# Performance work log

Hardware: AMD Instinct MI355X
Metric: run time of the kernel (lower is better)

## Reference

```python
import jax, jax.numpy as jnp
import numpy as np


def setup_inputs() -> dict:
    key = jax.random.key(0)
    k1, k2, k3, k4 = jax.random.split(key, 4)
    B, N, F, H, O = 4, 2048, 256, 8, 256
    nodes = jax.random.normal(k1, (B, N, F), dtype=jnp.float32)
    W_heads = jax.random.normal(k2, (H, F, F), dtype=jnp.float32) * (1.0 / np.sqrt(F))
    W_out = jax.random.normal(k3, (H * F, O), dtype=jnp.float32) * (1.0 / np.sqrt(H * F))
    bias = jax.random.normal(k4, (O,), dtype=jnp.float32) * 0.02
    return {"nodes": nodes, "W_heads": W_heads, "W_out": W_out, "bias": bias}


def reference(nodes, W_heads, W_out, bias):
    # nodes: [B,N,F]; W_heads: [H,F,F]; W_out: [H*F,O]; bias: [O]
    B, N, F = nodes.shape
    H = W_heads.shape[0]
    norm = 1.0 / jnp.sqrt(jnp.asarray(F, dtype=nodes.dtype))
    # per-head bilinear scores: (x @ W_h) @ x^T  -> [B,H,N,N]
    xw = jnp.einsum('bnf,hfg->bhng', nodes, W_heads)
    scores = jnp.einsum('bhng,bmg->bhnm', xw, nodes) * norm
    att = jax.nn.softmax(scores, axis=-1)
    # messages: att @ x (V = input nodes) -> [B,H,N,F]
    msgs = jnp.einsum('bhnm,bmf->bhnf', att, nodes)
    # concat heads along feature axis (head 0 first) -> [B,N,H*F]
    msgs = msgs.transpose(0, 2, 1, 3).reshape(B, N, H * F)
    return jnp.matmul(msgs, W_out) + bias
```

## Files before the change

kernel.cpp:

```cpp
#include <hip/hip_runtime.h>
#include <hip/hip_bf16.h>

#define B_ 4
#define N_ 2048
#define F_ 256
#define H_ 8
#define O_ 256

#define SCALE_QK 0.09016844005556021f

typedef __attribute__((ext_vector_type(8))) short short8;
typedef __attribute__((ext_vector_type(4))) short s16x4;
typedef __attribute__((ext_vector_type(4))) float f32x4;
typedef __attribute__((ext_vector_type(4))) unsigned int u32x4;

static __device__ __forceinline__ float bf2f(short u) {
    unsigned int x = ((unsigned int)(unsigned short)u) << 16;
    return __builtin_bit_cast(float, x);
}
static __device__ __forceinline__ short f2bf(float f) {
    unsigned int x = __builtin_bit_cast(unsigned int, f);
    unsigned int lsb = (x >> 16) & 1u;
    x += 0x7fffu + lsb;
    return (short)(x >> 16);
}
static __device__ __forceinline__ unsigned int pkbf(float a, float b) {
    return (unsigned int)(unsigned short)f2bf(a) |
           ((unsigned int)(unsigned short)f2bf(b) << 16);
}

static __device__ __forceinline__ void gld16(const short* g, short* l) {
    __builtin_amdgcn_global_load_lds(
        (const __attribute__((address_space(1))) void*)g,
        (__attribute__((address_space(3))) void*)l, 16, 0, 0);
}

__global__ __launch_bounds__(256) void cvtT_kernel(const float* __restrict__ src,
                                                   short* __restrict__ dst,
                                                   int R, int C) {
    __shared__ short tile[32][33];
    src += (size_t)blockIdx.z * R * C;
    dst += (size_t)blockIdx.z * R * C;
    int tx = threadIdx.x, ty = threadIdx.y;
    int c0 = blockIdx.x * 32, r0 = blockIdx.y * 32;
#pragma unroll
    for (int j = 0; j < 4; j++) {
        int r = r0 + ty + j * 8;
        tile[ty + j * 8][tx] = f2bf(src[(size_t)r * C + c0 + tx]);
    }
    __syncthreads();
#pragma unroll
    for (int j = 0; j < 4; j++) {
        int c = c0 + ty + j * 8;
        dst[(size_t)c * R + r0 + tx] = tile[tx][ty + j * 8];
    }
}

__global__ __launch_bounds__(256) void cvt_kernel(const float* __restrict__ src,
                                                  short* __restrict__ dst, int n) {
    int i = blockIdx.x * 256 + threadIdx.x;
    if (n >= 2048) {
        size_t base = (size_t)i * 8;
#pragma unroll
        for (int j = 0; j < 8; j++) dst[base + j] = f2bf(src[base + j]);
    } else if (i < n) {
        dst[i] = f2bf(src[i]);
    }
}

template <int NCT>
__device__ __forceinline__ void gemm64_bt(const short* __restrict__ A, int lda,
                                          const short* __restrict__ Bt, int ldb,
                                          float* __restrict__ C, int ldc,
                                          int K, const short* __restrict__ bias) {
    __shared__ short sA[64][72];
    __shared__ short sB[NCT * 16][72];
    int tid = threadIdx.x;
    int w = tid >> 6, l = tid & 63, lq = l & 15, quad = l >> 4;
    f32x4 acc[NCT];
#pragma unroll
    for (int i = 0; i < NCT; i++) acc[i] = (f32x4)(0.f);

    for (int kb = 0; kb < K; kb += 64) {
        __syncthreads();
#pragma unroll
        for (int i = 0; i < 2; i++) {
            int idx = tid + i * 256; int r = idx >> 3, c = (idx & 7) * 8;
            *(short8*)&sA[r][c] = *(const short8*)&A[(size_t)r * lda + kb + c];
        }
#pragma unroll
        for (int i = 0; i < NCT / 2; i++) {
            int idx = tid + i * 256; int r = idx >> 3, c = (idx & 7) * 8;
            *(short8*)&sB[r][c] = *(const short8*)&Bt[(size_t)r * ldb + kb + c];
        }
        __syncthreads();
#pragma unroll
        for (int kk = 0; kk < 2; kk++) {
            short8 af = *(const short8*)&sA[w * 16 + lq][kk * 32 + quad * 8];
#pragma unroll
            for (int ct = 0; ct < NCT; ct++) {
                short8 bf = *(const short8*)&sB[ct * 16 + lq][kk * 32 + quad * 8];
                acc[ct] = __builtin_amdgcn_mfma_f32_16x16x32_bf16(af, bf, acc[ct], 0, 0, 0);
            }
        }
    }
#pragma unroll
    for (int ct = 0; ct < NCT; ct++) {
        int col = ct * 16 + lq;
        float bv = bias ? bf2f(bias[col]) : 0.f;
#pragma unroll
        for (int r = 0; r < 4; r++) {
            int row = w * 16 + quad * 4 + r;
            C[(size_t)row * ldc + col] = acc[ct][r] + bv;
        }
    }
}

__global__ __launch_bounds__(256) void out_kernel(const short* __restrict__ msgs,
                                                  const short* __restrict__ WoutT,
                                                  const short* __restrict__ bias,
                                                  float* __restrict__ out) {
    int mt = blockIdx.x, nt = blockIdx.y;
    gemm64_bt<4>(msgs + (size_t)mt * 64 * (H_ * F_), H_ * F_,
                 WoutT + (size_t)nt * 64 * (H_ * F_), H_ * F_,
                 out + (size_t)mt * 64 * O_ + nt * 64, O_,
                 H_ * F_, bias + nt * 64);
}


#define STAGE_KV(KT, KVF, KVTF) do {                                         \
    _Pragma("unroll")                                                        \
    for (int i_ = 0; i_ < 4; i_++) {                                         \
        int rk_ = w * 8 + i_ * 2 + (l >> 5);                                 \
        int bk_ = (l & 31) ^ (rk_ & 31);                                     \
        gld16(&Xb[(size_t)((KT) * 64 + rk_) * F_ + bk_ * 8],                 \
              &KVF[(w * 8 + i_ * 2) * 256]);                                 \
        int rt_ = w * 32 + i_ * 8 + (l >> 3);                                \
        int bt_ = (l & 7) ^ (rt_ & 7);                                       \
        gld16(&XTb[(size_t)rt_ * N_ + (KT) * 64 + bt_ * 8],                  \
              &KVTF[(w * 32 + i_ * 8) * 64]);                                \
    }                                                                        \
} while (0)

#define COMPUTE_KT(KVF, KVTF) do {                                           \
    f32x4 sacc[4];                                                           \
    _Pragma("unroll")                                                        \
    for (int ct = 0; ct < 4; ct++) sacc[ct] = (f32x4)(0.f);                  \
    _Pragma("unroll")                                                        \
    for (int kk = 0; kk < 8; kk++) {                                         \
        _Pragma("unroll")                                                    \
        for (int ct = 0; ct < 4; ct++) {                                     \
            int arow = ct * 16 + lq;                                         \
            int ab = (kk * 4 + quad) ^ (arow & 31);                          \
            short8 af = *(const short8*)&KVF[arow * 256 + ab * 8];           \
            sacc[ct] = __builtin_amdgcn_mfma_f32_16x16x32_bf16(af, aq[kk], sacc[ct], 0, 0, 0); \
        }                                                                    \
    }                                                                        \
    float mx = -INFINITY;                                                    \
    _Pragma("unroll")                                                        \
    for (int ct = 0; ct < 4; ct++)                                           \
        _Pragma("unroll")                                                    \
        for (int r_ = 0; r_ < 4; r_++) mx = fmaxf(mx, sacc[ct][r_]);         \
    mx = fmaxf(mx, __shfl_xor(mx, 16));                                      \
    mx = fmaxf(mx, __shfl_xor(mx, 32));                                      \
    float mn = fmaxf(m_q, mx);                                               \
    float alpha = exp2f(m_q - mn);                                           \
    m_q = mn;                                                                \
    float pv[4][4]; float s_ = 0.f;                                          \
    _Pragma("unroll")                                                        \
    for (int ct = 0; ct < 4; ct++)                                           \
        _Pragma("unroll")                                                    \
        for (int r_ = 0; r_ < 4; r_++) {                                     \
            pv[ct][r_] = exp2f(sacc[ct][r_] - mn);                           \
            s_ += pv[ct][r_];                                                \
        }                                                                    \
    s_ += __shfl_xor(s_, 16);                                                \
    s_ += __shfl_xor(s_, 32);                                                \
    l_q = l_q * alpha + s_;                                                  \
    if (!__all(alpha == 1.0f)) {                                             \
        _Pragma("unroll")                                                    \
        for (int ct = 0; ct < 16; ct++)                                      \
            _Pragma("unroll")                                                \
            for (int r_ = 0; r_ < 4; r_++) oacc[ct][r_] *= alpha;            \
    }                                                                        \
    unsigned int w2[4][2];                                                   \
    _Pragma("unroll")                                                        \
    for (int ct = 0; ct < 4; ct++) {                                         \
        w2[ct][0] = pkbf(pv[ct][0], pv[ct][1]);                              \
        w2[ct][1] = pkbf(pv[ct][2], pv[ct][3]);                              \
    }                                                                        \
    int sl0 = (2 * (quad & 1)) * 16 + lq;                                    \
    int sl1 = sl0 + 16;                                                      \
    bool hi = (quad >> 1) != 0;                                              \
    short8 pfrag[2];                                                         \
    _Pragma("unroll")                                                        \
    for (int kk = 0; kk < 2; kk++) {                                         \
        unsigned int u0 = __shfl((int)w2[2 * kk][0], sl0);                   \
        unsigned int u1 = __shfl((int)w2[2 * kk][1], sl0);                   \
        unsigned int u2 = __shfl((int)w2[2 * kk][0], sl1);                   \
        unsigned int u3 = __shfl((int)w2[2 * kk][1], sl1);                   \
        unsigned int v0 = __shfl((int)w2[2 * kk + 1][0], sl0);               \
        unsigned int v1 = __shfl((int)w2[2 * kk + 1][1], sl0);               \
        unsigned int v2 = __shfl((int)w2[2 * kk + 1][0], sl1);               \
        unsigned int v3 = __shfl((int)w2[2 * kk + 1][1], sl1);               \
        u32x4 pk = { hi ? v0 : u0, hi ? v1 : u1, hi ? v2 : u2, hi ? v3 : u3 }; \
        pfrag[kk] = __builtin_bit_cast(short8, pk);                          \
    }                                                                        \
    _Pragma("unroll")                                                        \
    for (int ct = 0; ct < 16; ct++) {                                        \
        int arow = ct * 16 + lq;                                             \
        short8 a0 = *(const short8*)&KVTF[arow * 64 + ((quad) ^ (arow & 7)) * 8]; \
        short8 a1 = *(const short8*)&KVTF[arow * 64 + ((4 + quad) ^ (arow & 7)) * 8]; \
        oacc[ct] = __builtin_amdgcn_mfma_f32_16x16x32_bf16(a0, pfrag[0], oacc[ct], 0, 0, 0); \
        oacc[ct] = __builtin_amdgcn_mfma_f32_16x16x32_bf16(a1, pfrag[1], oacc[ct], 0, 0, 0); \
    }                                                                        \
} while (0)

__global__ __launch_bounds__(512) void attn_kernel(const short* __restrict__ X,
                                                   const short* __restrict__ WhT,
                                                   const short* __restrict__ XT,
                                                   short* __restrict__ msgs) {
    __shared__ short kvfA[64 * 256];
    __shared__ short kvfB[64 * 256];
    __shared__ short kvTfA[256 * 64];
    __shared__ short kvTfB[256 * 64];

    int qt = blockIdx.x, bh = blockIdx.y, b = bh >> 3, h = bh & 7;
    int tid = threadIdx.x, w = tid >> 6, l = tid & 63, lq = l & 15, quad = l >> 4;
    int q0 = qt * 128;

    const short* Xb  = X  + (size_t)b * N_ * F_;
    const short* XTb = XT + (size_t)b * F_ * N_;
    const short* Whh = WhT + (size_t)h * F_ * F_;

    f32x4 oacc[16];
    short8 aq[8];

#pragma unroll
    for (int i = 0; i < 16; i++) oacc[i] = (f32x4)(0.f);
    {
        short* xdst = (w < 4) ? kvfA : kvfB;
        int wl = w & 3;
#pragma unroll
        for (int i = 0; i < 8; i++) {
            int r = wl * 16 + i * 2 + (l >> 5);
            int bb = (l & 31) ^ (r & 31);
            gld16(&Xb[(size_t)(q0 + ((w >> 2) * 64) + r) * F_ + bb * 8],
                  &xdst[(wl * 16 + i * 2) * 256]);
        }
    }
    const short* xsrc = (w < 4) ? kvfA : kvfB;
#pragma unroll 1
    for (int kb = 0; kb < 4; kb++) {
        __syncthreads();
#pragma unroll
        for (int i = 0; i < 4; i++) {
            int rt = w * 32 + i * 8 + (l >> 3);
            int bt = (l & 7) ^ (rt & 7);
            gld16(&Whh[(size_t)rt * F_ + kb * 64 + bt * 8], &kvTfA[(w * 32 + i * 8) * 64]);
        }
        __syncthreads();
#pragma unroll
        for (int kk = 0; kk < 2; kk++) {
            int arow = (w & 3) * 16 + lq;
            int ab = (kb * 8 + kk * 4 + quad) ^ (arow & 31);
            short8 af = *(const short8*)&xsrc[arow * 256 + ab * 8];
#pragma unroll
            for (int ct = 0; ct < 16; ct++) {
                int brow = ct * 16 + lq;
                int bb = (kk * 4 + quad) ^ (brow & 7);
                short8 bf = *(const short8*)&kvTfA[brow * 64 + bb * 8];
                oacc[ct] = __builtin_amdgcn_mfma_f32_16x16x32_bf16(af, bf, oacc[ct], 0, 0, 0);
            }
        }
    }
    __syncthreads();
    {
        short* qdst = (w < 4) ? kvTfA : kvTfB;
#pragma unroll
        for (int ct = 0; ct < 16; ct++) {
#pragma unroll
            for (int r = 0; r < 4; r++) {
                int row = (w & 3) * 16 + quad * 4 + r;
                int col = ct * 16 + lq;
                int pb = (col >> 3) ^ (row & 31);
                qdst[row * 256 + pb * 8 + (col & 7)] = f2bf(oacc[ct][r] * SCALE_QK);
            }
        }
        __syncthreads();
#pragma unroll
        for (int kk = 0; kk < 8; kk++) {
            int row = (w & 3) * 16 + lq;
            int ab = (kk * 4 + quad) ^ (row & 31);
            aq[kk] = *(const short8*)&qdst[row * 256 + ab * 8];
        }
    }
    __syncthreads();

#pragma unroll
    for (int i = 0; i < 16; i++) oacc[i] = (f32x4)(0.f);
    float m_q = -INFINITY, l_q = 0.f;

    STAGE_KV(0, kvfA, kvTfA);
    __syncthreads();

#pragma unroll 1
    for (int kt2 = 0; kt2 < 16; kt2++) {
        STAGE_KV(2 * kt2 + 1, kvfB, kvTfB);
        COMPUTE_KT(kvfA, kvTfA);
        __syncthreads();
        STAGE_KV((2 * kt2 + 2) & 31, kvfA, kvTfA);
        COMPUTE_KT(kvfB, kvTfB);
        __syncthreads();
    }

    float inv = 1.f / l_q;
    short* Mout = msgs + (size_t)(b * N_ + q0 + w * 16 + lq) * (H_ * F_) + h * F_;
#pragma unroll
    for (int ct = 0; ct < 16; ct++) {
        s16x4 v4 = { f2bf(oacc[ct][0] * inv), f2bf(oacc[ct][1] * inv),
                     f2bf(oacc[ct][2] * inv), f2bf(oacc[ct][3] * inv) };
        *(s16x4*)&Mout[ct * 16 + quad * 4] = v4;
    }
}

extern "C" void kernel_launch(void* const* d_in, const int* in_sizes, int n_in,
                              void* d_out, int out_size, void* d_ws, size_t ws_size,
                              hipStream_t stream) {
    const float* nodes = (const float*)d_in[0];
    const float* Wh    = (const float*)d_in[1];
    const float* Wout  = (const float*)d_in[2];
    const float* bias  = (const float*)d_in[3];
    float* out = (float*)d_out;

    char* ws = (char*)d_ws;
    short* msgs   = (short*)(ws);
    short* WhT    = (short*)(ws + 33554432);
    short* WoutT  = (short*)(ws + 34603008);
    short* XT     = (short*)(ws + 35651584);
    short* Xbf    = (short*)(ws + 39845888);
    short* biasbf = (short*)(ws + 44040192);

    dim3 tblk(32, 8, 1);
    hipLaunchKernelGGL(cvtT_kernel, dim3(8, 8, 8),  tblk, 0, stream, Wh,    WhT,   256,  256);
    hipLaunchKernelGGL(cvtT_kernel, dim3(8, 64, 1), tblk, 0, stream, Wout,  WoutT, 2048, 256);
    hipLaunchKernelGGL(cvtT_kernel, dim3(8, 64, 4), tblk, 0, stream, nodes, XT,    2048, 256);
    hipLaunchKernelGGL(cvt_kernel,  dim3(1024), dim3(256), 0, stream, nodes, Xbf, 2097152);
    hipLaunchKernelGGL(cvt_kernel,  dim3(1),    dim3(256), 0, stream, bias, biasbf, 256);

    hipLaunchKernelGGL(attn_kernel, dim3(16, 32), dim3(512), 0, stream, Xbf, WhT, XT, msgs);
    hipLaunchKernelGGL(out_kernel,  dim3(128, 4), dim3(256), 0, stream, msgs, WoutT, biasbf, out);
}
```

Measured before the change: 293.3 us.

## Overlap KV staging with partial waitcnt, add MFMA priority, fuse node conversion

The attention K/V loop becomes a single 32-iteration loop that issues the next tile's async global-to-LDS loads, then waits only on the older loads (vmcnt(8)) before a raw s_barrier. The previous full __syncthreads drain is gone, so prefetch can overlap compute. MFMA sections are wrapped in s_setprio(1)/(0) so waves in matrix math get issue priority. Separately, the transpose-conversion kernel for nodes now also writes the untransposed bf16 copy, removing one launch and one extra read of the fp32 inputs. The risk is correctness of the hand-written waitcnt count and barrier placement.

```diff
diff --git a/kernel.cpp b/kernel.cpp
--- a/kernel.cpp
+++ b/kernel.cpp
@@ -36,36 +36,34 @@
 }
 
 __global__ __launch_bounds__(256) void cvtT_kernel(const float* __restrict__ src,
-                                                   short* __restrict__ dst,
+                                                   short* __restrict__ dstT,
+                                                   short* __restrict__ dst2,
                                                    int R, int C) {
     __shared__ short tile[32][33];
-    src += (size_t)blockIdx.z * R * C;
-    dst += (size_t)blockIdx.z * R * C;
+    src  += (size_t)blockIdx.z * R * C;
+    dstT += (size_t)blockIdx.z * R * C;
+    if (dst2) dst2 += (size_t)blockIdx.z * R * C;
     int tx = threadIdx.x, ty = threadIdx.y;
     int c0 = blockIdx.x * 32, r0 = blockIdx.y * 32;
 #pragma unroll
     for (int j = 0; j < 4; j++) {
         int r = r0 + ty + j * 8;
-        tile[ty + j * 8][tx] = f2bf(src[(size_t)r * C + c0 + tx]);
+        short v = f2bf(src[(size_t)r * C + c0 + tx]);
+        tile[ty + j * 8][tx] = v;
+        if (dst2) dst2[(size_t)r * C + c0 + tx] = v;
     }
     __syncthreads();
 #pragma unroll
     for (int j = 0; j < 4; j++) {
         int c = c0 + ty + j * 8;
-        dst[(size_t)c * R + r0 + tx] = tile[tx][ty + j * 8];
+        dstT[(size_t)c * R + r0 + tx] = tile[tx][ty + j * 8];
     }
 }
 
 __global__ __launch_bounds__(256) void cvt_kernel(const float* __restrict__ src,
                                                   short* __restrict__ dst, int n) {
     int i = blockIdx.x * 256 + threadIdx.x;
-    if (n >= 2048) {
-        size_t base = (size_t)i * 8;
-#pragma unroll
-        for (int j = 0; j < 8; j++) dst[base + j] = f2bf(src[base + j]);
-    } else if (i < n) {
-        dst[i] = f2bf(src[i]);
-    }
+    if (i < n) dst[i] = f2bf(src[i]);
 }
 
 template <int NCT>
@@ -146,6 +144,7 @@
     f32x4 sacc[4];                                                           \
     _Pragma("unroll")                                                        \
     for (int ct = 0; ct < 4; ct++) sacc[ct] = (f32x4)(0.f);                  \
+    __builtin_amdgcn_s_setprio(1);                                           \
     _Pragma("unroll")                                                        \
     for (int kk = 0; kk < 8; kk++) {                                         \
         _Pragma("unroll")                                                    \
@@ -156,6 +155,7 @@
             sacc[ct] = __builtin_amdgcn_mfma_f32_16x16x32_bf16(af, aq[kk], sacc[ct], 0, 0, 0); \
         }                                                                    \
     }                                                                        \
+    __builtin_amdgcn_s_setprio(0);                                           \
     float mx = -INFINITY;                                                    \
     _Pragma("unroll")                                                        \
     for (int ct = 0; ct < 4; ct++)                                           \
@@ -206,6 +206,7 @@
         u32x4 pk = { hi ? v0 : u0, hi ? v1 : u1, hi ? v2 : u2, hi ? v3 : u3 }; \
         pfrag[kk] = __builtin_bit_cast(short8, pk);                          \
     }                                                                        \
+    __builtin_amdgcn_s_setprio(1);                                           \
     _Pragma("unroll")                                                        \
     for (int ct = 0; ct < 16; ct++) {                                        \
         int arow = ct * 16 + lq;                                             \
@@ -214,6 +215,7 @@
         oacc[ct] = __builtin_amdgcn_mfma_f32_16x16x32_bf16(a0, pfrag[0], oacc[ct], 0, 0, 0); \
         oacc[ct] = __builtin_amdgcn_mfma_f32_16x16x32_bf16(a1, pfrag[1], oacc[ct], 0, 0, 0); \
     }                                                                        \
+    __builtin_amdgcn_s_setprio(0);                                           \
 } while (0)
 
 __global__ __launch_bounds__(512) void attn_kernel(const short* __restrict__ X,
@@ -302,16 +304,22 @@
     float m_q = -INFINITY, l_q = 0.f;
 
     STAGE_KV(0, kvfA, kvTfA);
-    __syncthreads();
 
 #pragma unroll 1
-    for (int kt2 = 0; kt2 < 16; kt2++) {
-        STAGE_KV(2 * kt2 + 1, kvfB, kvTfB);
-        COMPUTE_KT(kvfA, kvTfA);
-        __syncthreads();
-        STAGE_KV((2 * kt2 + 2) & 31, kvfA, kvTfA);
-        COMPUTE_KT(kvfB, kvTfB);
-        __syncthreads();
+    for (int kt = 0; kt < 32; kt++) {
+        const short* KVF  = (kt & 1) ? kvfB  : kvfA;
+        const short* KVTF = (kt & 1) ? kvTfB : kvTfA;
+        short* nKVF  = (kt & 1) ? kvfA  : kvfB;
+        short* nKVTF = (kt & 1) ? kvTfA : kvTfB;
+        STAGE_KV((kt + 1) & 31, nKVF, nKVTF);
+        asm volatile("s_waitcnt vmcnt(8)" ::: "memory");
+        __builtin_amdgcn_sched_barrier(0);
+        __builtin_amdgcn_s_barrier();
+        __builtin_amdgcn_sched_barrier(0);
+        COMPUTE_KT(KVF, KVTF);
+        __builtin_amdgcn_sched_barrier(0);
+        __builtin_amdgcn_s_barrier();
+        __builtin_amdgcn_sched_barrier(0);
     }
 
     float inv = 1.f / l_q;
@@ -342,10 +350,9 @@
     short* biasbf = (short*)(ws + 44040192);
 
     dim3 tblk(32, 8, 1);
-    hipLaunchKernelGGL(cvtT_kernel, dim3(8, 8, 8),  tblk, 0, stream, Wh,    WhT,   256,  256);
-    hipLaunchKernelGGL(cvtT_kernel, dim3(8, 64, 1), tblk, 0, stream, Wout,  WoutT, 2048, 256);
-    hipLaunchKernelGGL(cvtT_kernel, dim3(8, 64, 4), tblk, 0, stream, nodes, XT,    2048, 256);
-    hipLaunchKernelGGL(cvt_kernel,  dim3(1024), dim3(256), 0, stream, nodes, Xbf, 2097152);
+    hipLaunchKernelGGL(cvtT_kernel, dim3(8, 8, 8),  tblk, 0, stream, Wh,    WhT,   (short*)nullptr, 256,  256);
+    hipLaunchKernelGGL(cvtT_kernel, dim3(8, 64, 1), tblk, 0, stream, Wout,  WoutT, (short*)nullptr, 2048, 256);
+    hipLaunchKernelGGL(cvtT_kernel, dim3(8, 64, 4), tblk, 0, stream, nodes, XT,    Xbf,             2048, 256);
     hipLaunchKernelGGL(cvt_kernel,  dim3(1),    dim3(256), 0, stream, bias, biasbf, 256);
 
     hipLaunchKernelGGL(attn_kernel, dim3(16, 32), dim3(512), 0, stream, Xbf, WhT, XT, msgs);
```

After: 343.5 us. +17.1%, slower.
